# Optimization experiments

Hardware: AMD Instinct MI355X
Metric: run time of the kernel (lower is better)

## Reference

```python
import jax, jax.numpy as jnp
import numpy as np

NUM_CLASSES = 21
EPS = 1e-6


def setup_inputs() -> dict:
    key = jax.random.key(0)
    k1, k2, k3 = jax.random.split(key, 3)
    feats = jax.random.normal(k1, (8, 256, 64, 64), dtype=jnp.float32)
    preds = jax.random.normal(k2, (8, NUM_CLASSES, 256, 256), dtype=jnp.float32)
    # labels in [0, 22): includes nclass=21 which acts as an ignore label
    masks = jax.random.randint(k3, (8, 256, 256), 0, 22, dtype=jnp.int64)
    return {"feats": feats, "preds": preds, "masks": masks}


def reference(feats, preds, masks):
    B, C = feats.shape[0], feats.shape[1]
    H, W = masks.shape[-2:]
    K = NUM_CLASSES

    # argmax over class logits -> predicted label map [B, H, W]
    pred_lbl = jnp.argmax(preds, axis=1)

    # bilinear upsample (align_corners=False, matches half-pixel resize)
    feats_up = jax.image.resize(feats, (B, C, H, W), method="bilinear")

    cls = jnp.arange(K)
    # one-hot of gt mask and of predictions; labels >= K (incl. 255) fall in
    # the dropped last channel of one_hot_2d, i.e. match no class here.
    gt_oh = (masks[:, None, :, :] == cls[None, :, None, None])      # [B,K,H,W]
    pr_oh = (pred_lbl[:, None, :, :] == cls[None, :, None, None])   # [B,K,H,W]
    joint = (gt_oh & pr_oh).astype(feats_up.dtype)                  # [B,K,H,W]

    counts = joint.sum(axis=(2, 3))                                  # [B,K]
    sums = jnp.einsum("bchw,bkhw->bkc", feats_up, joint)            # [B,K,C]

    # per-image class means (absent classes -> 0/eps = 0), then batch mean
    proto = (sums / (counts[..., None] + EPS)).mean(axis=0)          # [K,C]
    return proto
```

## Files before the change

### kernel.cpp

```cpp
#include <hip/hip_runtime.h>

#define KC   21
#define BB   8
#define CC   256
#define HWP  65536
#define SRC  4096
#define NS   128
#define PC   32

#define WSF_PARTW 131072
#define WSF_PART  (WSF_PARTW + BB*NS*KC)

__global__ __launch_bounds__(256, 2)
void k1_classify(const float* __restrict__ preds,
                 const int*   __restrict__ masks,
                 unsigned char* __restrict__ L,
                 float* __restrict__ out)
{
    int tid = threadIdx.x;
    if (blockIdx.x == 0) {
        float4* o4 = reinterpret_cast<float4*>(out);
#pragma unroll
        for (int i = 0; i < (KC * CC / 4 + 255) / 256; ++i) {
            int j = tid + i * 256;
            if (j < KC * CC / 4) o4[j] = make_float4(0.f, 0.f, 0.f, 0.f);
        }
    }

    int idx = blockIdx.x * 256 + tid;
    int b   = idx >> 14;
    int hw4 = (idx & 16383) << 2;

    const float* pb = preds + (size_t)b * KC * HWP + hw4;
    float va[4][KC];
#pragma unroll
    for (int k = 0; k < KC; ++k) {
        float4 t = *reinterpret_cast<const float4*>(pb + (size_t)k * HWP);
        va[0][k] = t.x; va[1][k] = t.y; va[2][k] = t.z; va[3][k] = t.w;
    }

    int4 mm = *reinterpret_cast<const int4*>(masks + b * HWP + hw4);
    int mk[4] = { mm.x, mm.y, mm.z, mm.w };

    uchar4 r;
    unsigned char* rp = reinterpret_cast<unsigned char*>(&r);
#pragma unroll
    for (int j = 0; j < 4; ++j) {
        float best = va[j][0];
        int   bi   = 0;
#pragma unroll
        for (int k = 1; k < KC; ++k) {
            if (va[j][k] > best) { best = va[j][k]; bi = k; }
        }
        rp[j] = (mk[j] == bi) ? (unsigned char)bi : (unsigned char)255;
    }
    *reinterpret_cast<uchar4*>(L + (size_t)b * HWP + hw4) = r;
}

__global__ __launch_bounds__(512, 8)
void k2_contract(const float* __restrict__ feats,
                 const unsigned char* __restrict__ L,
                 float* __restrict__ partial,
                 float* __restrict__ partialw)
{
    __shared__ float ws[KC * PC];
    __shared__ float scr[KC * CC];
    int s = blockIdx.x, b = blockIdx.y;
    int tid = threadIdx.x;
    int y = s >> 1, x0c = (s & 1) * PC;
    int p0 = y * 64 + x0c;

    int cp   = tid & 255;
    int psub = tid >> 8;
    int pw   = psub * 16;

    if (tid < KC * PC / 4)
        *reinterpret_cast<float4*>(ws + tid * 4) = make_float4(0.f, 0.f, 0.f, 0.f);

    float f[16];
    {
        const float* frow = feats + (size_t)(b * CC + cp) * SRC + p0 + pw;
#pragma unroll
        for (int q = 0; q < 4; ++q) {
            float4 t = *reinterpret_cast<const float4*>(frow + q * 4);
            f[q * 4 + 0] = t.x; f[q * 4 + 1] = t.y;
            f[q * 4 + 2] = t.z; f[q * 4 + 3] = t.w;
        }
    }
    __syncthreads();

    {
        int r = tid >> 6, cb = tid & 63;
        int h = 4 * y - 2 + r;
        if ((unsigned)h < 256u) {
            float sy = h * 0.25f - 0.375f;
            int   yt = (int)floorf(sy);
            float wy = sy - (float)yt;
            int ya = yt < 0 ? 0 : yt;
            int yb = yt + 1 > 63 ? 63 : yt + 1;
            float wyy = ((ya == y) ? (1.f - wy) : 0.f) + ((yb == y) ? wy : 0.f);
            if (wyy != 0.f) {
                const unsigned char* Lrow = L + ((size_t)b << 16) + ((size_t)h << 8);
                int wb0 = 4 * x0c - 2;
#pragma unroll
                for (int j = 0; j < 3; ++j) {
                    int col = cb + j * 64;
                    int w = wb0 + col;
                    if (col < 136 && (unsigned)w < 256u) {
                        int k = Lrow[w];
                        if (k < KC) {
                            float sx = w * 0.25f - 0.375f;
                            int   xt = (int)floorf(sx);
                            float wx = sx - (float)xt;
                            int xa = xt < 0 ? 0 : xt;
                            int xb = xt + 1 > 63 ? 63 : xt + 1;
                            if (xa >= x0c && xa < x0c + PC)
                                atomicAdd(&ws[k * PC + xa - x0c], wyy * (1.f - wx));
                            if (xb >= x0c && xb < x0c + PC)
                                atomicAdd(&ws[k * PC + xb - x0c], wyy * wx);
                        }
                    }
                }
            }
        }
    }
    __syncthreads();

    float swcnt = 0.f;
    if (tid < KC) {
#pragma unroll
        for (int p = 0; p < PC; ++p) swcnt += ws[tid * PC + ((p + tid) & (PC - 1))];
    }

    float acc[KC];
#pragma unroll
    for (int k = 0; k < KC; ++k) {
        const float* wk = ws + k * PC + pw;
        float a0 = 0.f, a1 = 0.f, a2 = 0.f, a3 = 0.f;
#pragma unroll
        for (int q = 0; q < 4; ++q) {
            float4 w4 = *reinterpret_cast<const float4*>(wk + q * 4);
            a0 += w4.x * f[q * 4 + 0];
            a1 += w4.y * f[q * 4 + 1];
            a2 += w4.z * f[q * 4 + 2];
            a3 += w4.w * f[q * 4 + 3];
        }
        acc[k] = (a0 + a1) + (a2 + a3);
    }

    if (psub == 1) {
#pragma unroll
        for (int k = 0; k < KC; ++k) scr[k * CC + cp] = acc[k];
    }
    __syncthreads();
    if (psub == 0) {
        float* op = partial + ((size_t)(b * NS + s)) * KC * CC + cp;
#pragma unroll
        for (int k = 0; k < KC; ++k)
            op[(size_t)k * CC] = acc[k] + scr[k * CC + cp];
    }

    if (tid < KC)
        partialw[(size_t)(b * NS + s) * KC + tid] = swcnt;
}

__global__ __launch_bounds__(256)
void k3_finalize(const float* __restrict__ partial,
                 const float* __restrict__ partialw,
                 float* __restrict__ out)
{
    int k = blockIdx.x, b = blockIdx.y;
    int tid = threadIdx.x;

    const float* base = partial + ((size_t)(b * NS) * KC + k) * CC + tid;
    float acc = 0.f;
#pragma unroll 8
    for (int s = 0; s < NS; ++s) acc += base[(size_t)s * KC * CC];

    __shared__ float red[2];
    float v = 0.f;
    if (tid < NS) v = partialw[(size_t)(b * NS + tid) * KC + k];
#pragma unroll
    for (int off = 32; off; off >>= 1) v += __shfl_down(v, off);
    if (tid < NS && (tid & 63) == 0) red[tid >> 6] = v;
    __syncthreads();
    float cnt = red[0] + red[1];

    atomicAdd(&out[k * CC + tid], acc / (8.f * (cnt + 1e-6f)));
}

extern "C" void kernel_launch(void* const* d_in, const int* in_sizes, int n_in,
                              void* d_out, int out_size, void* d_ws, size_t ws_size,
                              hipStream_t stream) {
    const float* feats = (const float*)d_in[0];
    const float* preds = (const float*)d_in[1];
    const int*   masks = (const int*)  d_in[2];
    float* out = (float*)d_out;

    float* wsf = (float*)d_ws;
    unsigned char* L = (unsigned char*)d_ws;
    float* partialw = wsf + WSF_PARTW;
    float* partial  = wsf + WSF_PART;

    k1_classify<<<(BB * HWP / 4) / 256, 256, 0, stream>>>(preds, masks, L, out);
    k2_contract<<<dim3(NS, BB), 512, 0, stream>>>(feats, L, partial, partialw);
    k3_finalize<<<dim3(KC, BB), 256, 0, stream>>>(partial, partialw, out);
}
```

Measured before the change: 36.67 us.

## Split weight-map construction into separate kernel and simplify contraction

Moves the transposed-bilinear splat of the joint label map into a new kernel that writes a per-image, per-class weight map on the 64x64 source grid into global memory, one block per source row, so halo rows are processed once per row instead of once per half-row tile. Per-class counts are now accumulated with global atomics, replacing the separate partial-count buffer and its reduction in the finalize kernel. The contraction kernel becomes a plain 256-thread kernel that reads the weights from global (L2-cached) memory instead of shared memory, with no shared-memory staging or cross-half reduction. The cost is an extra kernel launch and a global write and read of the weight map.

Measured after the change: 44.61 us. 1.22x slower.

```diff
diff --git a/kernel.cpp b/kernel.cpp
--- a/kernel.cpp
+++ b/kernel.cpp
@@ -8,14 +8,16 @@
 #define NS   128
 #define PC   32
 
-#define WSF_PARTW 131072
-#define WSF_PART  (WSF_PARTW + BB*NS*KC)
+#define WSF_COUNTS 131072
+#define WSF_PART   (WSF_COUNTS + 256)
+#define WSF_WG     8388608
 
 __global__ __launch_bounds__(256, 2)
 void k1_classify(const float* __restrict__ preds,
                  const int*   __restrict__ masks,
                  unsigned char* __restrict__ L,
-                 float* __restrict__ out)
+                 float* __restrict__ out,
+                 float* __restrict__ counts)
 {
     int tid = threadIdx.x;
     if (blockIdx.x == 0) {
@@ -25,6 +27,8 @@
             int j = tid + i * 256;
             if (j < KC * CC / 4) o4[j] = make_float4(0.f, 0.f, 0.f, 0.f);
         }
+        if (tid < 64)
+            reinterpret_cast<float4*>(counts)[tid] = make_float4(0.f, 0.f, 0.f, 0.f);
     }
 
     int idx = blockIdx.x * 256 + tid;
@@ -38,7 +42,6 @@
         float4 t = *reinterpret_cast<const float4*>(pb + (size_t)k * HWP);
         va[0][k] = t.x; va[1][k] = t.y; va[2][k] = t.z; va[3][k] = t.w;
     }
-
     int4 mm = *reinterpret_cast<const int4*>(masks + b * HWP + hw4);
     int mk[4] = { mm.x, mm.y, mm.z, mm.w };
 
@@ -49,48 +52,28 @@
         float best = va[j][0];
         int   bi   = 0;
 #pragma unroll
-        for (int k = 1; k < KC; ++k) {
+        for (int k = 1; k < KC; ++k)
             if (va[j][k] > best) { best = va[j][k]; bi = k; }
-        }
         rp[j] = (mk[j] == bi) ? (unsigned char)bi : (unsigned char)255;
     }
     *reinterpret_cast<uchar4*>(L + (size_t)b * HWP + hw4) = r;
 }
 
-__global__ __launch_bounds__(512, 8)
-void k2_contract(const float* __restrict__ feats,
-                 const unsigned char* __restrict__ L,
-                 float* __restrict__ partial,
-                 float* __restrict__ partialw)
+__global__ __launch_bounds__(256)
+void kW_build(const unsigned char* __restrict__ L,
+              float* __restrict__ Wg,
+              float* __restrict__ counts)
 {
-    __shared__ float ws[KC * PC];
-    __shared__ float scr[KC * CC];
-    int s = blockIdx.x, b = blockIdx.y;
+    __shared__ float ws[KC * 64];
+    int y = blockIdx.x, b = blockIdx.y;
     int tid = threadIdx.x;
-    int y = s >> 1, x0c = (s & 1) * PC;
-    int p0 = y * 64 + x0c;
 
-    int cp   = tid & 255;
-    int psub = tid >> 8;
-    int pw   = psub * 16;
-
-    if (tid < KC * PC / 4)
-        *reinterpret_cast<float4*>(ws + tid * 4) = make_float4(0.f, 0.f, 0.f, 0.f);
-
-    float f[16];
-    {
-        const float* frow = feats + (size_t)(b * CC + cp) * SRC + p0 + pw;
-#pragma unroll
-        for (int q = 0; q < 4; ++q) {
-            float4 t = *reinterpret_cast<const float4*>(frow + q * 4);
-            f[q * 4 + 0] = t.x; f[q * 4 + 1] = t.y;
-            f[q * 4 + 2] = t.z; f[q * 4 + 3] = t.w;
-        }
-    }
+    for (int t = tid; t < KC * 16; t += 256)
+        *reinterpret_cast<float4*>(ws + t * 4) = make_float4(0.f, 0.f, 0.f, 0.f);
     __syncthreads();
 
     {
-        int r = tid >> 6, cb = tid & 63;
+        int r = tid >> 5, cb = tid & 31;
         int h = 4 * y - 2 + r;
         if ((unsigned)h < 256u) {
             float sy = h * 0.25f - 0.375f;
@@ -101,24 +84,18 @@
             float wyy = ((ya == y) ? (1.f - wy) : 0.f) + ((yb == y) ? wy : 0.f);
             if (wyy != 0.f) {
                 const unsigned char* Lrow = L + ((size_t)b << 16) + ((size_t)h << 8);
-                int wb0 = 4 * x0c - 2;
 #pragma unroll
-                for (int j = 0; j < 3; ++j) {
-                    int col = cb + j * 64;
-                    int w = wb0 + col;
-                    if (col < 136 && (unsigned)w < 256u) {
-                        int k = Lrow[w];
-                        if (k < KC) {
-                            float sx = w * 0.25f - 0.375f;
-                            int   xt = (int)floorf(sx);
-                            float wx = sx - (float)xt;
-                            int xa = xt < 0 ? 0 : xt;
-                            int xb = xt + 1 > 63 ? 63 : xt + 1;
-                            if (xa >= x0c && xa < x0c + PC)
-                                atomicAdd(&ws[k * PC + xa - x0c], wyy * (1.f - wx));
-                            if (xb >= x0c && xb < x0c + PC)
-                                atomicAdd(&ws[k * PC + xb - x0c], wyy * wx);
-                        }
+                for (int j = 0; j < 8; ++j) {
+                    int w = cb + j * 32;
+                    int k = Lrow[w];
+                    if (k < KC) {
+                        float sx = w * 0.25f - 0.375f;
+                        int   xt = (int)floorf(sx);
+                        float wx = sx - (float)xt;
+                        int xa = xt < 0 ? 0 : xt;
+                        int xb = xt + 1 > 63 ? 63 : xt + 1;
+                        atomicAdd(&ws[k * 64 + xa], wyy * (1.f - wx));
+                        atomicAdd(&ws[k * 64 + xb], wyy * wx);
                     }
                 }
             }
@@ -126,47 +103,63 @@
     }
     __syncthreads();
 
-    float swcnt = 0.f;
     if (tid < KC) {
+        float sw = 0.f;
 #pragma unroll
-        for (int p = 0; p < PC; ++p) swcnt += ws[tid * PC + ((p + tid) & (PC - 1))];
+        for (int x = 0; x < 64; ++x) sw += ws[tid * 64 + ((x + tid) & 63)];
+        if (sw != 0.f) atomicAdd(&counts[b * KC + tid], sw);
     }
 
-    float acc[KC];
+    for (int t = tid; t < KC * 16; t += 256) {
+        int k = t >> 4, q = t & 15;
+        *reinterpret_cast<float4*>(Wg + (size_t)(b * KC + k) * SRC + y * 64 + q * 4) =
+            *reinterpret_cast<const float4*>(ws + k * 64 + q * 4);
+    }
+}
+
+__global__ __launch_bounds__(256, 4)
+void k2_contract(const float* __restrict__ feats,
+                 const float* __restrict__ Wg,
+                 float* __restrict__ partial)
+{
+    int s = blockIdx.x, b = blockIdx.y;
+    int c = threadIdx.x;
+    int p0 = s * PC;
+
+    float f[PC];
+    {
+        const float* frow = feats + (size_t)(b * CC + c) * SRC + p0;
 #pragma unroll
+        for (int q = 0; q < PC / 4; ++q) {
+            float4 t = *reinterpret_cast<const float4*>(frow + q * 4);
+            f[q * 4 + 0] = t.x; f[q * 4 + 1] = t.y;
+            f[q * 4 + 2] = t.z; f[q * 4 + 3] = t.w;
+        }
+    }
+
+    const float* wb = Wg + (size_t)b * KC * SRC + p0;
+    float* op = partial + ((size_t)(b * NS + s)) * KC * CC + c;
+
+#pragma unroll 3
     for (int k = 0; k < KC; ++k) {
-        const float* wk = ws + k * PC + pw;
+        const float* wk = wb + (size_t)k * SRC;
         float a0 = 0.f, a1 = 0.f, a2 = 0.f, a3 = 0.f;
 #pragma unroll
-        for (int q = 0; q < 4; ++q) {
-            float4 w4 = *reinterpret_cast<const float4*>(wk + q * 4);
-            a0 += w4.x * f[q * 4 + 0];
-            a1 += w4.y * f[q * 4 + 1];
-            a2 += w4.z * f[q * 4 + 2];
-            a3 += w4.w * f[q * 4 + 3];
+        for (int q = 0; q < PC / 4; ++q) {
+            float w0 = wk[q * 4 + 0], w1 = wk[q * 4 + 1];
+            float w2 = wk[q * 4 + 2], w3 = wk[q * 4 + 3];
+            a0 += w0 * f[q * 4 + 0];
+            a1 += w1 * f[q * 4 + 1];
+            a2 += w2 * f[q * 4 + 2];
+            a3 += w3 * f[q * 4 + 3];
         }
-        acc[k] = (a0 + a1) + (a2 + a3);
+        op[(size_t)k * CC] = (a0 + a1) + (a2 + a3);
     }
-
-    if (psub == 1) {
-#pragma unroll
-        for (int k = 0; k < KC; ++k) scr[k * CC + cp] = acc[k];
-    }
-    __syncthreads();
-    if (psub == 0) {
-        float* op = partial + ((size_t)(b * NS + s)) * KC * CC + cp;
-#pragma unroll
-        for (int k = 0; k < KC; ++k)
-            op[(size_t)k * CC] = acc[k] + scr[k * CC + cp];
-    }
-
-    if (tid < KC)
-        partialw[(size_t)(b * NS + s) * KC + tid] = swcnt;
 }
 
 __global__ __launch_bounds__(256)
 void k3_finalize(const float* __restrict__ partial,
-                 const float* __restrict__ partialw,
+                 const float* __restrict__ counts,
                  float* __restrict__ out)
 {
     int k = blockIdx.x, b = blockIdx.y;
@@ -177,15 +170,7 @@
 #pragma unroll 8
     for (int s = 0; s < NS; ++s) acc += base[(size_t)s * KC * CC];
 
-    __shared__ float red[2];
-    float v = 0.f;
-    if (tid < NS) v = partialw[(size_t)(b * NS + tid) * KC + k];
-#pragma unroll
-    for (int off = 32; off; off >>= 1) v += __shfl_down(v, off);
-    if (tid < NS && (tid & 63) == 0) red[tid >> 6] = v;
-    __syncthreads();
-    float cnt = red[0] + red[1];
-
+    float cnt = counts[b * KC + k];
     atomicAdd(&out[k * CC + tid], acc / (8.f * (cnt + 1e-6f)));
 }
 
@@ -199,10 +184,12 @@
 
     float* wsf = (float*)d_ws;
     unsigned char* L = (unsigned char*)d_ws;
-    float* partialw = wsf + WSF_PARTW;
-    float* partial  = wsf + WSF_PART;
+    float* counts  = wsf + WSF_COUNTS;
+    float* partial = wsf + WSF_PART;
+    float* Wg      = wsf + WSF_WG;
 
-    k1_classify<<<(BB * HWP / 4) / 256, 256, 0, stream>>>(preds, masks, L, out);
-    k2_contract<<<dim3(NS, BB), 512, 0, stream>>>(feats, L, partial, partialw);
-    k3_finalize<<<dim3(KC, BB), 256, 0, stream>>>(partial, partialw, out);
+    k1_classify<<<(BB * HWP / 4) / 256, 256, 0, stream>>>(preds, masks, L, out, counts);
+    kW_build<<<dim3(64, BB), 256, 0, stream>>>(L, Wg, counts);
+    k2_contract<<<dim3(NS, BB), 256, 0, stream>>>(feats, Wg, partial);
+    k3_finalize<<<dim3(KC, BB), 256, 0, stream>>>(partial, counts, out);
 }
```

## Enlarge contract tiles to two source rows and finalize without atomics

Applied to the files above, without the earlier changes.

The contraction kernel now gives each block two full 64-pixel source rows, 128 pixels in all. It runs 256 threads, each owning one channel, and loops over four 32-pixel chunks instead of splitting pixels across half-blocks and reducing through shared memory. This cuts the partial-sum count per image from 128 to 32, which shrinks partial writes and the finalize reads. The finalize kernel now loops over the batch inside one block per class and writes the output directly, so the output zeroing in the classify kernel and the global atomics are gone. The trade-off is fewer blocks in the contraction kernel (256 instead of 1024), which lowers parallelism and latency hiding, and more serial work per thread in finalize.

Result: slower. 63.72 us (+73.8%).

```diff
diff --git a/kernel.cpp b/kernel.cpp
--- a/kernel.cpp
+++ b/kernel.cpp
@@ -5,28 +5,17 @@
 #define CC   256
 #define HWP  65536
 #define SRC  4096
-#define NS   128
-#define PC   32
+#define NS2  32
 
 #define WSF_PARTW 131072
-#define WSF_PART  (WSF_PARTW + BB*NS*KC)
+#define WSF_PART  139264
 
 __global__ __launch_bounds__(256, 2)
 void k1_classify(const float* __restrict__ preds,
                  const int*   __restrict__ masks,
-                 unsigned char* __restrict__ L,
-                 float* __restrict__ out)
+                 unsigned char* __restrict__ L)
 {
     int tid = threadIdx.x;
-    if (blockIdx.x == 0) {
-        float4* o4 = reinterpret_cast<float4*>(out);
-#pragma unroll
-        for (int i = 0; i < (KC * CC / 4 + 255) / 256; ++i) {
-            int j = tid + i * 256;
-            if (j < KC * CC / 4) o4[j] = make_float4(0.f, 0.f, 0.f, 0.f);
-        }
-    }
-
     int idx = blockIdx.x * 256 + tid;
     int b   = idx >> 14;
     int hw4 = (idx & 16383) << 2;
@@ -38,7 +27,6 @@
         float4 t = *reinterpret_cast<const float4*>(pb + (size_t)k * HWP);
         va[0][k] = t.x; va[1][k] = t.y; va[2][k] = t.z; va[3][k] = t.w;
     }
-
     int4 mm = *reinterpret_cast<const int4*>(masks + b * HWP + hw4);
     int mk[4] = { mm.x, mm.y, mm.z, mm.w };
 
@@ -49,64 +37,47 @@
         float best = va[j][0];
         int   bi   = 0;
 #pragma unroll
-        for (int k = 1; k < KC; ++k) {
+        for (int k = 1; k < KC; ++k)
             if (va[j][k] > best) { best = va[j][k]; bi = k; }
-        }
         rp[j] = (mk[j] == bi) ? (unsigned char)bi : (unsigned char)255;
     }
     *reinterpret_cast<uchar4*>(L + (size_t)b * HWP + hw4) = r;
 }
 
-__global__ __launch_bounds__(512, 8)
+__global__ __launch_bounds__(256)
 void k2_contract(const float* __restrict__ feats,
                  const unsigned char* __restrict__ L,
                  float* __restrict__ partial,
                  float* __restrict__ partialw)
 {
-    __shared__ float ws[KC * PC];
-    __shared__ float scr[KC * CC];
+    __shared__ float ws[KC * 128];
     int s = blockIdx.x, b = blockIdx.y;
     int tid = threadIdx.x;
-    int y = s >> 1, x0c = (s & 1) * PC;
-    int p0 = y * 64 + x0c;
+    int p0 = s * 128;
+    int ybase = 2 * s;
 
-    int cp   = tid & 255;
-    int psub = tid >> 8;
-    int pw   = psub * 16;
-
-    if (tid < KC * PC / 4)
-        *reinterpret_cast<float4*>(ws + tid * 4) = make_float4(0.f, 0.f, 0.f, 0.f);
-
-    float f[16];
-    {
-        const float* frow = feats + (size_t)(b * CC + cp) * SRC + p0 + pw;
-#pragma unroll
-        for (int q = 0; q < 4; ++q) {
-            float4 t = *reinterpret_cast<const float4*>(frow + q * 4);
-            f[q * 4 + 0] = t.x; f[q * 4 + 1] = t.y;
-            f[q * 4 + 2] = t.z; f[q * 4 + 3] = t.w;
-        }
-    }
+    for (int t = tid; t < KC * 32; t += 256)
+        *reinterpret_cast<float4*>(ws + t * 4) = make_float4(0.f, 0.f, 0.f, 0.f);
     __syncthreads();
 
     {
-        int r = tid >> 6, cb = tid & 63;
-        int h = 4 * y - 2 + r;
-        if ((unsigned)h < 256u) {
-            float sy = h * 0.25f - 0.375f;
-            int   yt = (int)floorf(sy);
-            float wy = sy - (float)yt;
-            int ya = yt < 0 ? 0 : yt;
-            int yb = yt + 1 > 63 ? 63 : yt + 1;
-            float wyy = ((ya == y) ? (1.f - wy) : 0.f) + ((yb == y) ? wy : 0.f);
-            if (wyy != 0.f) {
-                const unsigned char* Lrow = L + ((size_t)b << 16) + ((size_t)h << 8);
-                int wb0 = 4 * x0c - 2;
+        int r4 = tid >> 6, cb = tid & 63;
 #pragma unroll
-                for (int j = 0; j < 3; ++j) {
-                    int col = cb + j * 64;
-                    int w = wb0 + col;
-                    if (col < 136 && (unsigned)w < 256u) {
+        for (int rr = 0; rr < 3; ++rr) {
+            int h = 8 * s - 2 + rr * 4 + r4;
+            if ((unsigned)h < 256u) {
+                float sy = h * 0.25f - 0.375f;
+                int   yt = (int)floorf(sy);
+                float wy = sy - (float)yt;
+                int ya = yt < 0 ? 0 : yt;
+                int yb = yt + 1 > 63 ? 63 : yt + 1;
+                float wyy0 = ((ya == ybase)     ? (1.f - wy) : 0.f) + ((yb == ybase)     ? wy : 0.f);
+                float wyy1 = ((ya == ybase + 1) ? (1.f - wy) : 0.f) + ((yb == ybase + 1) ? wy : 0.f);
+                if (wyy0 != 0.f || wyy1 != 0.f) {
+                    const unsigned char* Lrow = L + ((size_t)b << 16) + ((size_t)h << 8);
+#pragma unroll
+                    for (int j = 0; j < 4; ++j) {
+                        int w = cb + j * 64;
                         int k = Lrow[w];
                         if (k < KC) {
                             float sx = w * 0.25f - 0.375f;
@@ -114,10 +85,15 @@
                             float wx = sx - (float)xt;
                             int xa = xt < 0 ? 0 : xt;
                             int xb = xt + 1 > 63 ? 63 : xt + 1;
-                            if (xa >= x0c && xa < x0c + PC)
-                                atomicAdd(&ws[k * PC + xa - x0c], wyy * (1.f - wx));
-                            if (xb >= x0c && xb < x0c + PC)
-                                atomicAdd(&ws[k * PC + xb - x0c], wyy * wx);
+                            float* wk = ws + k * 128;
+                            if (wyy0 != 0.f) {
+                                atomicAdd(wk + xa, wyy0 * (1.f - wx));
+                                atomicAdd(wk + xb, wyy0 * wx);
+                            }
+                            if (wyy1 != 0.f) {
+                                atomicAdd(wk + 64 + xa, wyy1 * (1.f - wx));
+                                atomicAdd(wk + 64 + xb, wyy1 * wx);
+                            }
                         }
                     }
                 }
@@ -129,39 +105,47 @@
     float swcnt = 0.f;
     if (tid < KC) {
 #pragma unroll
-        for (int p = 0; p < PC; ++p) swcnt += ws[tid * PC + ((p + tid) & (PC - 1))];
+        for (int i = 0; i < 128; ++i)
+            swcnt += ws[tid * 128 + ((i + tid * 8) & 127)];
     }
 
     float acc[KC];
 #pragma unroll
-    for (int k = 0; k < KC; ++k) {
-        const float* wk = ws + k * PC + pw;
-        float a0 = 0.f, a1 = 0.f, a2 = 0.f, a3 = 0.f;
+    for (int k = 0; k < KC; ++k) acc[k] = 0.f;
+
+    const float* frow = feats + (size_t)(b * CC + tid) * SRC + p0;
 #pragma unroll
-        for (int q = 0; q < 4; ++q) {
-            float4 w4 = *reinterpret_cast<const float4*>(wk + q * 4);
-            a0 += w4.x * f[q * 4 + 0];
-            a1 += w4.y * f[q * 4 + 1];
-            a2 += w4.z * f[q * 4 + 2];
-            a3 += w4.w * f[q * 4 + 3];
+    for (int ss = 0; ss < 4; ++ss) {
+        float f[32];
+#pragma unroll
+        for (int q = 0; q < 8; ++q) {
+            float4 t = *reinterpret_cast<const float4*>(frow + ss * 32 + q * 4);
+            f[q * 4 + 0] = t.x; f[q * 4 + 1] = t.y;
+            f[q * 4 + 2] = t.z; f[q * 4 + 3] = t.w;
         }
-        acc[k] = (a0 + a1) + (a2 + a3);
+#pragma unroll
+        for (int k = 0; k < KC; ++k) {
+            const float* wk = ws + k * 128 + ss * 32;
+            float a0 = 0.f, a1 = 0.f, a2 = 0.f, a3 = 0.f;
+#pragma unroll
+            for (int q = 0; q < 8; ++q) {
+                float4 w4 = *reinterpret_cast<const float4*>(wk + q * 4);
+                a0 += w4.x * f[q * 4 + 0];
+                a1 += w4.y * f[q * 4 + 1];
+                a2 += w4.z * f[q * 4 + 2];
+                a3 += w4.w * f[q * 4 + 3];
+            }
+            acc[k] += (a0 + a1) + (a2 + a3);
+        }
     }
 
-    if (psub == 1) {
+    float* op = partial + ((size_t)(b * NS2 + s) * KC) * CC + tid;
 #pragma unroll
-        for (int k = 0; k < KC; ++k) scr[k * CC + cp] = acc[k];
-    }
-    __syncthreads();
-    if (psub == 0) {
-        float* op = partial + ((size_t)(b * NS + s)) * KC * CC + cp;
-#pragma unroll
-        for (int k = 0; k < KC; ++k)
-            op[(size_t)k * CC] = acc[k] + scr[k * CC + cp];
-    }
+    for (int k = 0; k < KC; ++k)
+        op[(size_t)k * CC] = acc[k];
 
     if (tid < KC)
-        partialw[(size_t)(b * NS + s) * KC + tid] = swcnt;
+        partialw[(b * NS2 + s) * KC + tid] = swcnt;
 }
 
 __global__ __launch_bounds__(256)
@@ -169,24 +153,25 @@
                  const float* __restrict__ partialw,
                  float* __restrict__ out)
 {
-    int k = blockIdx.x, b = blockIdx.y;
-    int tid = threadIdx.x;
+    int k = blockIdx.x;
+    int c = threadIdx.x;
 
-    const float* base = partial + ((size_t)(b * NS) * KC + k) * CC + tid;
-    float acc = 0.f;
+    float r = 0.f;
+#pragma unroll 1
+    for (int b = 0; b < BB; ++b) {
+        float cnt = 0.f;
+#pragma unroll
+        for (int s = 0; s < NS2; ++s)
+            cnt += partialw[(b * NS2 + s) * KC + k];
+
+        float acc = 0.f;
+        const float* base = partial + ((size_t)(b * NS2) * KC + k) * CC + c;
 #pragma unroll 8
-    for (int s = 0; s < NS; ++s) acc += base[(size_t)s * KC * CC];
+        for (int s = 0; s < NS2; ++s) acc += base[(size_t)s * KC * CC];
 
-    __shared__ float red[2];
-    float v = 0.f;
-    if (tid < NS) v = partialw[(size_t)(b * NS + tid) * KC + k];
-#pragma unroll
-    for (int off = 32; off; off >>= 1) v += __shfl_down(v, off);
-    if (tid < NS && (tid & 63) == 0) red[tid >> 6] = v;
-    __syncthreads();
-    float cnt = red[0] + red[1];
-
-    atomicAdd(&out[k * CC + tid], acc / (8.f * (cnt + 1e-6f)));
+        r += acc / (cnt + 1e-6f);
+    }
+    out[k * CC + c] = r * 0.125f;
 }
 
 extern "C" void kernel_launch(void* const* d_in, const int* in_sizes, int n_in,
@@ -202,7 +187,7 @@
     float* partialw = wsf + WSF_PARTW;
     float* partial  = wsf + WSF_PART;
 
-    k1_classify<<<(BB * HWP / 4) / 256, 256, 0, stream>>>(preds, masks, L, out);
-    k2_contract<<<dim3(NS, BB), 512, 0, stream>>>(feats, L, partial, partialw);
-    k3_finalize<<<dim3(KC, BB), 256, 0, stream>>>(partial, partialw, out);
+    k1_classify<<<(BB * HWP / 4) / 256, 256, 0, stream>>>(preds, masks, L);
+    k2_contract<<<dim3(NS2, BB), 256, 0, stream>>>(feats, L, partial, partialw);
+    k3_finalize<<<KC, 256, 0, stream>>>(partial, partialw, out);
 }
```
